# Kernel optimization log

Measured on AMD Instinct MI355X. Metric: run time of the kernel, lower is better.

## Reference

```python
import jax, jax.numpy as jnp
import numpy as np
import math

B, S, D, H = 2, 2048, 1024, 16
DPH = D // H  # 64

def setup_inputs() -> dict:
    key = jax.random.key(0)
    ks = jax.random.split(key, 13)
    scale = 1.0 / math.sqrt(D)
    inp = {
        'key': jax.random.normal(ks[0], (B, S, D), jnp.float32),
        'value': jax.random.normal(ks[1], (B, S, D), jnp.float32),
        'query': jax.random.normal(ks[2], (B, S, D), jnp.float32),
        # binary mask [B, q_len, k_len]; True = disallowed (masked_fill with -inf)
        'mask': jax.random.randint(ks[3], (B, S, S), 0, 2).astype(bool),
        'Wq': jax.random.normal(ks[4], (D, D), jnp.float32) * scale,
        'bq': jnp.zeros((D,), jnp.float32),
        'Wk': jax.random.normal(ks[5], (D, D), jnp.float32) * scale,
        'bk': jnp.zeros((D,), jnp.float32),
        'Wv': jax.random.normal(ks[6], (D, D), jnp.float32) * scale,
        'bv': jnp.zeros((D,), jnp.float32),
        'Wo': jax.random.normal(ks[7], (D, D), jnp.float32) * scale,
        'bo': jnp.zeros((D,), jnp.float32),
    }
    return inp

def _shape(x):
    # [B, S, D] -> [B, H, S, DPH]
    return x.reshape(B, -1, H, DPH).transpose(0, 2, 1, 3)

def reference(key, value, query, mask, Wq, bq, Wk, bk, Wv, bv, Wo, bo):
    k = _shape(key @ Wk + bk)      # [B,H,S,DPH]
    v = _shape(value @ Wv + bv)    # [B,H,S,DPH]
    q = _shape(query @ Wq + bq)    # [B,H,S,DPH]
    q = q / math.sqrt(DPH)
    scores = jnp.einsum('bhqd,bhkd->bhqk', q, k)   # [B,H,S,S]
    scores = jnp.where(mask[:, None, :, :], -jnp.inf, scores)
    attn = jax.nn.softmax(scores, axis=-1)
    # dropout is identity in eval / p=0
    ctx = jnp.einsum('bhqk,bhkd->bhqd', attn, v)   # [B,H,S,DPH]
    ctx = ctx.transpose(0, 2, 1, 3).reshape(B, -1, D)
    return ctx @ Wo + bo
```

## Files before the change

kernel.cpp:

```cpp
#include <hip/hip_runtime.h>
#include <hip/hip_bf16.h>
#include <cstdint>

#define B_   2
#define S_   2048
#define D_   1024
#define H_   16
#define DPH_ 64
#define NT_  (S_ / 64)

typedef float f32x4 __attribute__((ext_vector_type(4)));
typedef short bf16x8 __attribute__((ext_vector_type(8)));
typedef unsigned short u16;

static const size_t NE = (size_t)B_ * S_ * D_;
static const size_t DD = (size_t)D_ * D_;

__device__ __forceinline__ u16 f2bf(float f) {
  union { float f; unsigned u; } cv; cv.f = f;
  unsigned u = cv.u;
  return (u16)((u + 0x7fffu + ((u >> 16) & 1u)) >> 16);
}

__device__ __forceinline__ unsigned cvtpk(float a, float b) {
  unsigned r;
  asm("v_cvt_pk_bf16_f32 %0, %1, %2" : "=v"(r) : "v"(a), "v"(b));
  return r;
}

__device__ __forceinline__ void gld16(const void* g, void* l) {
  __builtin_amdgcn_global_load_lds((const __attribute__((address_space(1))) unsigned int*)g,
                                   (__attribute__((address_space(3))) unsigned int*)l, 16, 0, 0);
}

__global__ __launch_bounds__(256) void detect_mask_fmt(const uint4* __restrict__ m,
                                                       unsigned int* __restrict__ flags) {
  int i = blockIdx.x * 256 + threadIdx.x;
  uint4 v = m[i];
  int a = (v.x > 1u) | (v.y > 1u) | (v.z > 1u) | (v.w > 1u);
  int bb = ((v.x != 0u && v.x != 0x3f800000u) | (v.y != 0u && v.y != 0x3f800000u) |
            (v.z != 0u && v.z != 0x3f800000u) | (v.w != 0u && v.w != 0x3f800000u));
  int anyA = __any(a), anyB = __any(bb);
  if ((threadIdx.x & 63) == 0) {
    if (anyA) flags[0] = 1u;
    if (anyB) flags[1] = 1u;
  }
}

__device__ __forceinline__ unsigned nz4(unsigned w) {
  unsigned r = 0;
  if (w & 0x000000ffu) r |= 1u;
  if (w & 0x0000ff00u) r |= 2u;
  if (w & 0x00ff0000u) r |= 4u;
  if (w & 0xff000000u) r |= 8u;
  return r;
}

__global__ __launch_bounds__(256) void prep_bits(const void* __restrict__ src,
                                                 const unsigned int* __restrict__ flags,
                                                 unsigned long long* __restrict__ dst) {
  int i = blockIdx.x * 256 + threadIdx.x;
  unsigned long long w = 0;
  bool fourB = (flags[0] == 0u) || (flags[1] == 0u);
  if (fourB) {
    const uint4* p = (const uint4*)src + (size_t)i * 16;
#pragma unroll
    for (int j = 0; j < 16; ++j) {
      uint4 v = p[j];
      unsigned bits = (v.x ? 1u : 0u) | (v.y ? 2u : 0u) | (v.z ? 4u : 0u) | (v.w ? 8u : 0u);
      w |= (unsigned long long)bits << (j * 4);
    }
  } else {
    const uint4* p = (const uint4*)src + (size_t)i * 4;
#pragma unroll
    for (int j = 0; j < 4; ++j) {
      uint4 v = p[j];
      w |= (unsigned long long)nz4(v.x) << (j * 16 + 0);
      w |= (unsigned long long)nz4(v.y) << (j * 16 + 4);
      w |= (unsigned long long)nz4(v.z) << (j * 16 + 8);
      w |= (unsigned long long)nz4(v.w) << (j * 16 + 12);
    }
  }
  dst[i] = w;
}

__global__ __launch_bounds__(256) void cvt_w(const float* __restrict__ Wq, const float* __restrict__ Wk,
                                             const float* __restrict__ Wv, const float* __restrict__ Wo,
                                             u16* __restrict__ WT) {
  int idx2 = blockIdx.x;
  int mat = idx2 >> 9;
  const float* W = (mat == 0) ? Wq : (mat == 1) ? Wk : (mat == 2) ? Wv : Wo;
  u16* O = WT + (size_t)mat * DD;
  int t = (idx2 & 511) * 256 + threadIdx.x;
  int n = t & 1023, k8 = (t >> 10) << 3;
  bf16x8 o;
#pragma unroll
  for (int j = 0; j < 8; ++j) o[j] = (short)f2bf(W[(size_t)(k8 + j) * D_ + n]);
  *(bf16x8*)(O + (size_t)n * D_ + k8) = o;
}

struct GArgs {
  const void* A[3]; const u16* W[3]; const float* bias[3];
  void* C[3]; float scale[3]; int mode[3];
};

template <int AF32>
__global__ __launch_bounds__(256, 3) void gemm_bf16(GArgs ga) {
  __shared__ unsigned char smem[49152];
  constexpr int ABUF = AF32 ? 16384 : 8192;
  const int z = blockIdx.z;
  const u16* WT = ga.W[z]; const float* bias = ga.bias[z];
  void* Cout = ga.C[z]; const float scale = ga.scale[z]; const int mode = ga.mode[z];

  const int tid = threadIdx.x, wv = tid >> 6, lane = tid & 63;
  const int hi = lane >> 4, lo = lane & 15;
  const int wm = wv >> 1, wn = wv & 1;
  const int m0 = blockIdx.y * 128, n0 = blockIdx.x * 128;
  const char* ag = (const char*)ga.A[z] + (size_t)m0 * (AF32 ? 4096 : 2048);
  const char* bg = (const char*)WT + (size_t)n0 * 2048;
  unsigned char* sB0 = smem + 2 * ABUF;

  f32x4 acc[4][4];
#pragma unroll
  for (int i = 0; i < 4; ++i)
#pragma unroll
    for (int j = 0; j < 4; ++j) acc[i][j] = (f32x4){0.f, 0.f, 0.f, 0.f};

  auto stageA = [&](unsigned char* dst, int kt) {
    if constexpr (AF32) {
#pragma unroll
      for (int p = 0; p < 4; ++p) {
        int cid = p * 4 + wv;
        int slot = cid * 64 + lane;
        int r = slot >> 3, c = slot & 7;
        gld16(ag + (size_t)r * 4096 + kt * 128 + ((c ^ (r & 7)) * 16), dst + cid * 1024);
      }
    } else {
#pragma unroll
      for (int p = 0; p < 2; ++p) {
        int cid = p * 4 + wv;
        int slot = cid * 64 + lane;
        int r = slot >> 2, c = slot & 3;
        gld16(ag + (size_t)r * 2048 + kt * 64 + ((c ^ (r & 3)) * 16), dst + cid * 1024);
      }
    }
  };
  auto stageB = [&](unsigned char* dst, int kt) {
#pragma unroll
    for (int p = 0; p < 2; ++p) {
      int cid = p * 4 + wv;
      int slot = cid * 64 + lane;
      int r = slot >> 2, c = slot & 3;
      gld16(bg + (size_t)r * 2048 + kt * 64 + ((c ^ (r & 3)) * 16), dst + cid * 1024);
    }
  };

  stageA(smem, 0);
  stageB(sB0, 0);

  for (int kt = 0; kt < 32; ++kt) {
    int cur = kt & 1;
    unsigned char* sA = smem + cur * ABUF;
    unsigned char* sB = sB0 + cur * 8192;
    if (kt < 31) {
      stageA(smem + (cur ^ 1) * ABUF, kt + 1);
      stageB(sB0 + (cur ^ 1) * 8192, kt + 1);
      if constexpr (AF32) asm volatile("s_waitcnt vmcnt(6)" ::: "memory");
      else                asm volatile("s_waitcnt vmcnt(4)" ::: "memory");
    } else {
      asm volatile("s_waitcnt vmcnt(0)" ::: "memory");
    }
    __builtin_amdgcn_s_barrier();
    __builtin_amdgcn_sched_barrier(0);

    bf16x8 af[4], bf[4];
#pragma unroll
    for (int i = 0; i < 4; ++i) {
      int mr = 64 * wm + 16 * i + lo;
      if constexpr (AF32) {
        int s7 = mr & 7;
        f32x4 A0 = *(const f32x4*)(sA + mr * 128 + (((2 * hi) ^ s7) * 16));
        f32x4 A1 = *(const f32x4*)(sA + mr * 128 + (((2 * hi + 1) ^ s7) * 16));
        union { uint4 u; bf16x8 v; } cvu;
        cvu.u = make_uint4(cvtpk(A0[0], A0[1]), cvtpk(A0[2], A0[3]),
                           cvtpk(A1[0], A1[1]), cvtpk(A1[2], A1[3]));
        af[i] = cvu.v;
      } else {
        af[i] = *(const bf16x8*)(sA + mr * 64 + ((hi ^ (mr & 3)) * 16));
      }
      int nr = 64 * wn + 16 * i + lo;
      bf[i] = *(const bf16x8*)(sB + nr * 64 + ((hi ^ (nr & 3)) * 16));
    }
#pragma unroll
    for (int i = 0; i < 4; ++i)
#pragma unroll
      for (int j = 0; j < 4; ++j)
        acc[i][j] = __builtin_amdgcn_mfma_f32_16x16x32_bf16(af[i], bf[j], acc[i][j], 0, 0, 0);

    __builtin_amdgcn_sched_barrier(0);
    __builtin_amdgcn_s_barrier();
  }

  float bv[4];
#pragma unroll
  for (int j = 0; j < 4; ++j) bv[j] = bias[n0 + 64 * wn + 16 * j + lo];

  if (mode <= 1) {
#pragma unroll
    for (int i = 0; i < 4; ++i)
#pragma unroll
      for (int r = 0; r < 4; ++r) {
        int m = m0 + 64 * wm + 16 * i + 4 * hi + r;
#pragma unroll
        for (int j = 0; j < 4; ++j) {
          int n = n0 + 64 * wn + 16 * j + lo;
          float val = (acc[i][j][r] + bv[j]) * scale;
          if (mode == 0) ((u16*)Cout)[(size_t)m * D_ + n] = f2bf(val);
          else           ((float*)Cout)[(size_t)m * D_ + n] = val;
        }
      }
  } else {
    __syncthreads();
#pragma unroll
    for (int i = 0; i < 4; ++i) {
      int mb2 = 64 * wm + 16 * i + 4 * hi;
#pragma unroll
      for (int j = 0; j < 4; ++j) {
        int n = 64 * wn + 16 * j + lo;
        unsigned w0 = (unsigned)f2bf(acc[i][j][0] + bv[j]) | ((unsigned)f2bf(acc[i][j][1] + bv[j]) << 16);
        unsigned w1 = (unsigned)f2bf(acc[i][j][2] + bv[j]) | ((unsigned)f2bf(acc[i][j][3] + bv[j]) << 16);
        unsigned byteoff = n * 256 + ((2 * mb2) ^ ((n & 7) << 5));
        *(uint2*)(smem + byteoff) = make_uint2(w0, w1);
      }
    }
    __syncthreads();
    int nl = tid >> 1, half = tid & 1;
    unsigned ob[32];
#pragma unroll
    for (int s = 0; s < 16; ++s) {
      unsigned byteoff = nl * 256 + ((128 * half + 8 * s) ^ ((nl & 7) << 5));
      uint2 vv = *(const uint2*)(smem + byteoff);
      ob[2 * s] = vv.x; ob[2 * s + 1] = vv.y;
    }
    int bb = blockIdx.y >> 4;
    int habs = blockIdx.x * 2 + (nl >> 6);
    int dn = nl & 63;
    size_t sg = (size_t)(blockIdx.y & 15) * 128 + half * 64;
    u16* outp = (u16*)Cout + ((size_t)(bb * H_ + habs) * 64 + dn) * 2048 + sg;
#pragma unroll
    for (int c2 = 0; c2 < 8; ++c2)
      *(uint4*)(outp + c2 * 8) = *(uint4*)&ob[4 * c2];
  }
}

__global__ __launch_bounds__(256, 3) void attn_mfma3(const u16* __restrict__ Qb,
                                                     const u16* __restrict__ Kb,
                                                     const u16* __restrict__ VT,
                                                     const unsigned long long* __restrict__ M1,
                                                     u16* __restrict__ CTX) {
  __shared__ unsigned char sK[2][8192];
  __shared__ unsigned char sV[2][8192];
  __shared__ unsigned char sP[4][4096];
  const int tid = threadIdx.x, wv = tid >> 6, lane = tid & 63;
  const int hi = lane >> 4, lo = lane & 15;
  const int b = blockIdx.y >> 4, h = blockIdx.y & (H_ - 1);
  const int q0 = blockIdx.x * 128;
  const char* kg = (const char*)(Kb + (size_t)b * S_ * D_ + h * 64);
  const char* vg = (const char*)(VT + ((size_t)(b * H_ + h) * 64) * S_);
  unsigned* sPw = (unsigned*)sP[wv];

  const u16* qr0 = Qb + ((size_t)b * S_ + q0 + 32 * wv + lo) * D_ + h * 64;
  bf16x8 qa[2][2];
  qa[0][0] = *(const bf16x8*)(qr0 + 8 * hi);
  qa[0][1] = *(const bf16x8*)(qr0 + 32 + 8 * hi);
  qa[1][0] = *(const bf16x8*)(qr0 + (size_t)16 * D_ + 8 * hi);
  qa[1][1] = *(const bf16x8*)(qr0 + (size_t)16 * D_ + 32 + 8 * hi);

  auto stage8 = [&](unsigned char* dst, const char* srcbase, size_t rs) {
#pragma unroll
    for (int p = 0; p < 2; ++p) {
      int cid = p * 4 + wv;
      int slot = cid * 64 + lane;
      int r = slot >> 3, c = slot & 7;
      gld16(srcbase + (size_t)r * rs + ((c ^ (r & 7)) * 16), dst + cid * 1024);
    }
  };

  stage8(sK[0], kg, 2048);
  stage8(sV[0], vg, 4096);

  f32x4 acc[2][4];
#pragma unroll
  for (int hf = 0; hf < 2; ++hf)
#pragma unroll
    for (int i = 0; i < 4; ++i) acc[hf][i] = (f32x4){0.f, 0.f, 0.f, 0.f};
  float lrowp[2] = {0.f, 0.f};
  const unsigned long long* mrp = M1 + ((size_t)b * S_ + q0 + 32 * wv + lo) * NT_;

#define ATTN_STEP(CUR, KT)                                                             \
  {                                                                                    \
    if ((KT) < NT_ - 1) {                                                              \
      stage8(sK[(CUR) ^ 1], kg + (size_t)((KT) + 1) * 64 * 2048, 2048);                \
      stage8(sV[(CUR) ^ 1], vg + (size_t)((KT) + 1) * 128, 4096);                      \
      asm volatile("s_waitcnt vmcnt(4)" ::: "memory");                                 \
    } else {                                                                           \
      asm volatile("s_waitcnt vmcnt(0)" ::: "memory");                                 \
    }                                                                                  \
    __builtin_amdgcn_s_barrier();                                                      \
    __builtin_amdgcn_sched_barrier(0);                                                 \
    unsigned long long mwh0 = mrp[(KT)] >> (unsigned)(4 * hi);                         \
    unsigned long long mwh1 = mrp[(size_t)16 * NT_ + (KT)] >> (unsigned)(4 * hi);      \
    f32x4 sc[2][4];                                                                    \
    __builtin_amdgcn_s_setprio(1);                                                     \
    _Pragma("unroll")                                                                  \
    for (int nf = 0; nf < 4; ++nf) {                                                   \
      int key = 16 * nf + lo;                                                          \
      bf16x8 kb0 = *(const bf16x8*)(sK[(CUR)] + key * 128 + (((0 + hi) ^ (key & 7)) * 16)); \
      bf16x8 kb1 = *(const bf16x8*)(sK[(CUR)] + key * 128 + (((4 + hi) ^ (key & 7)) * 16)); \
      f32x4 z0 = (f32x4){0.f, 0.f, 0.f, 0.f};                                          \
      f32x4 z1 = (f32x4){0.f, 0.f, 0.f, 0.f};                                          \
      z0 = __builtin_amdgcn_mfma_f32_16x16x32_bf16(kb0, qa[0][0], z0, 0, 0, 0);        \
      z1 = __builtin_amdgcn_mfma_f32_16x16x32_bf16(kb0, qa[1][0], z1, 0, 0, 0);        \
      z0 = __builtin_amdgcn_mfma_f32_16x16x32_bf16(kb1, qa[0][1], z0, 0, 0, 0);        \
      z1 = __builtin_amdgcn_mfma_f32_16x16x32_bf16(kb1, qa[1][1], z1, 0, 0, 0);        \
      sc[0][nf] = z0; sc[1][nf] = z1;                                                  \
    }                                                                                  \
    __builtin_amdgcn_s_setprio(0);                                                     \
    _Pragma("unroll")                                                                  \
    for (int hf2 = 0; hf2 < 2; ++hf2) {                                                \
      unsigned long long mw = (hf2 == 0) ? mwh0 : mwh1;                                \
      unsigned nlo = ~(unsigned)mw;                                                    \
      unsigned nhi = ~(unsigned)(mw >> 32);                                            \
      float p[4][4];                                                                   \
      float rs = 0.f;                                                                  \
      _Pragma("unroll")                                                                \
      for (int nf = 0; nf < 4; ++nf) {                                                 \
        unsigned hfm = (nf < 2) ? nlo : nhi;                                           \
        _Pragma("unroll")                                                              \
        for (int r = 0; r < 4; ++r) {                                                  \
          float e = __builtin_amdgcn_exp2f(__builtin_fminf(sc[hf2][nf][r], 88.0f));    \
          int keep = ((int)(hfm << (31 - (16 * (nf & 1) + r)))) >> 31;                 \
          p[nf][r] = __uint_as_float(__float_as_uint(e) & (unsigned)keep);             \
        }                                                                              \
      }                                                                                \
      rs = ((p[0][0] + p[0][1]) + (p[0][2] + p[0][3])) +                               \
           ((p[1][0] + p[1][1]) + (p[1][2] + p[1][3])) +                               \
           ((p[2][0] + p[2][1]) + (p[2][2] + p[2][3])) +                               \
           ((p[3][0] + p[3][1]) + (p[3][2] + p[3][3]));                                \
      lrowp[hf2] += rs;                                                                \
      int rq = 16 * hf2 + lo;                                                          \
      _Pragma("unroll")                                                                \
      for (int nf = 0; nf < 4; ++nf) {                                                 \
        unsigned w0 = cvtpk(p[nf][0], p[nf][1]);                                       \
        unsigned w1 = cvtpk(p[nf][2], p[nf][3]);                                       \
        int dw = rq * 32 + ((8 * nf + 2 * hi) ^ ((lo & 7) << 2));                      \
        *(uint2*)(sPw + dw) = make_uint2(w0, w1);                                      \
      }                                                                                \
    }                                                                                  \
    __builtin_amdgcn_s_setprio(1);                                                     \
    _Pragma("unroll")                                                                  \
    for (int mh = 0; mh < 2; ++mh) {                                                   \
      bf16x8 pf0 = *(const bf16x8*)(sPw + (lo * 32 + ((16 * mh + 4 * hi) ^ ((lo & 7) << 2)))); \
      bf16x8 pf1 = *(const bf16x8*)(sPw + ((16 + lo) * 32 + ((16 * mh + 4 * hi) ^ ((lo & 7) << 2)))); \
      _Pragma("unroll")                                                                \
      for (int nd = 0; nd < 4; ++nd) {                                                 \
        int d = 16 * nd + lo;                                                          \
        bf16x8 vb = *(const bf16x8*)(sV[(CUR)] + d * 128 + (((4 * mh + hi) ^ (d & 7)) * 16)); \
        acc[0][nd] = __builtin_amdgcn_mfma_f32_16x16x32_bf16(vb, pf0, acc[0][nd], 0, 0, 0); \
        acc[1][nd] = __builtin_amdgcn_mfma_f32_16x16x32_bf16(vb, pf1, acc[1][nd], 0, 0, 0); \
      }                                                                                \
    }                                                                                  \
    __builtin_amdgcn_s_setprio(0);                                                     \
    __builtin_amdgcn_sched_barrier(0);                                                 \
    __builtin_amdgcn_s_barrier();                                                      \
  }

  for (int kt2 = 0; kt2 < NT_ / 2; ++kt2) {
    ATTN_STEP(0, 2 * kt2);
    ATTN_STEP(1, 2 * kt2 + 1);
  }
#undef ATTN_STEP

#pragma unroll
  for (int hf = 0; hf < 2; ++hf) {
    float lr = lrowp[hf];
    lr += __shfl_xor(lr, 16);
    lr += __shfl_xor(lr, 32);
    float inv = lr > 0.f ? 1.f / lr : 0.f;
    u16* crow = CTX + ((size_t)b * S_ + q0 + 32 * wv + 16 * hf + lo) * D_ + h * 64;
#pragma unroll
    for (int nd = 0; nd < 4; ++nd) {
      unsigned w0 = (unsigned)f2bf(acc[hf][nd][0] * inv) | ((unsigned)f2bf(acc[hf][nd][1] * inv) << 16);
      unsigned w1 = (unsigned)f2bf(acc[hf][nd][2] * inv) | ((unsigned)f2bf(acc[hf][nd][3] * inv) << 16);
      *(uint2*)(crow + 16 * nd + 4 * hi) = make_uint2(w0, w1);
    }
  }
}

extern "C" void kernel_launch(void* const* d_in, const int* in_sizes, int n_in,
                              void* d_out, int out_size, void* d_ws, size_t ws_size,
                              hipStream_t stream) {
  const float* key   = (const float*)d_in[0];
  const float* value = (const float*)d_in[1];
  const float* query = (const float*)d_in[2];
  const void*  mask  = d_in[3];
  const float* Wq = (const float*)d_in[4];
  const float* bq = (const float*)d_in[5];
  const float* Wk = (const float*)d_in[6];
  const float* bk = (const float*)d_in[7];
  const float* Wv = (const float*)d_in[8];
  const float* bv = (const float*)d_in[9];
  const float* Wo = (const float*)d_in[10];
  const float* bo = (const float*)d_in[11];

  u16* Qb  = (u16*)d_ws;
  u16* Kb  = Qb + NE;
  u16* VTb = Kb + NE;
  u16* WT  = VTb + NE;
  unsigned long long* M1 = (unsigned long long*)(WT + 4 * DD);
  unsigned int* flags = (unsigned int*)(M1 + (size_t)B_ * S_ * NT_);

  hipMemsetAsync(flags, 0, 8, stream);
  detect_mask_fmt<<<128, 256, 0, stream>>>((const uint4*)mask, flags);
  prep_bits<<<512, 256, 0, stream>>>(mask, flags, M1);
  cvt_w<<<2048, 256, 0, stream>>>(Wq, Wk, Wv, Wo, WT);

  const float QSCALE = 0.125f * 1.4426950408889634f;
  GArgs g3;
  g3.A[0] = query; g3.W[0] = WT + 0 * DD; g3.bias[0] = bq; g3.C[0] = Qb;  g3.scale[0] = QSCALE; g3.mode[0] = 0;
  g3.A[1] = key;   g3.W[1] = WT + 1 * DD; g3.bias[1] = bk; g3.C[1] = Kb;  g3.scale[1] = 1.f;    g3.mode[1] = 0;
  g3.A[2] = value; g3.W[2] = WT + 2 * DD; g3.bias[2] = bv; g3.C[2] = VTb; g3.scale[2] = 1.f;    g3.mode[2] = 2;
  gemm_bf16<1><<<dim3(D_ / 128, (B_ * S_) / 128, 3), 256, 0, stream>>>(g3);

  attn_mfma3<<<dim3(S_ / 128, B_ * H_), 256, 0, stream>>>(Qb, Kb, VTb, M1, Qb);

  GArgs go;
  go.A[0] = Qb; go.W[0] = WT + 3 * DD; go.bias[0] = bo; go.C[0] = d_out; go.scale[0] = 1.f; go.mode[0] = 1;
  go.A[1] = Qb; go.W[1] = WT + 3 * DD; go.bias[1] = bo; go.C[1] = d_out; go.scale[1] = 1.f; go.mode[1] = 1;
  go.A[2] = Qb; go.W[2] = WT + 3 * DD; go.bias[2] = bo; go.C[2] = d_out; go.scale[2] = 1.f; go.mode[2] = 1;
  gemm_bf16<0><<<dim3(D_ / 128, (B_ * S_) / 128, 1), 256, 0, stream>>>(go);
}
```

Baseline: 301.5 us.

## Halve attention query tile to 64 rows and swap GEMM grid rasterization

The attention kernel now processes 64 queries per block (16 per wave) instead of 128, shrinking registers and the P shared buffer so launch bounds can target 4 blocks per CU, and doubling the grid size. This aims to improve occupancy and load balance across CUs at the cost of staging each K/V tile twice as often per query. The projection GEMMs swap grid x/y so consecutive blocks iterate over M rows rather than N columns, changing L2 reuse of weights versus activations.

```diff
diff --git a/kernel.cpp b/kernel.cpp
--- a/kernel.cpp
+++ b/kernel.cpp
@@ -115,7 +115,7 @@
   const int tid = threadIdx.x, wv = tid >> 6, lane = tid & 63;
   const int hi = lane >> 4, lo = lane & 15;
   const int wm = wv >> 1, wn = wv & 1;
-  const int m0 = blockIdx.y * 128, n0 = blockIdx.x * 128;
+  const int m0 = blockIdx.x * 128, n0 = blockIdx.y * 128;
   const char* ag = (const char*)ga.A[z] + (size_t)m0 * (AF32 ? 4096 : 2048);
   const char* bg = (const char*)WT + (size_t)n0 * 2048;
   unsigned char* sB0 = smem + 2 * ABUF;
@@ -242,10 +242,10 @@
       uint2 vv = *(const uint2*)(smem + byteoff);
       ob[2 * s] = vv.x; ob[2 * s + 1] = vv.y;
     }
-    int bb = blockIdx.y >> 4;
-    int habs = blockIdx.x * 2 + (nl >> 6);
+    int bb = blockIdx.x >> 4;
+    int habs = blockIdx.y * 2 + (nl >> 6);
     int dn = nl & 63;
-    size_t sg = (size_t)(blockIdx.y & 15) * 128 + half * 64;
+    size_t sg = (size_t)(blockIdx.x & 15) * 128 + half * 64;
     u16* outp = (u16*)Cout + ((size_t)(bb * H_ + habs) * 64 + dn) * 2048 + sg;
 #pragma unroll
     for (int c2 = 0; c2 < 8; ++c2)
@@ -253,28 +253,25 @@
   }
 }
 
-__global__ __launch_bounds__(256, 3) void attn_mfma3(const u16* __restrict__ Qb,
+__global__ __launch_bounds__(256, 4) void attn_mfma4(const u16* __restrict__ Qb,
                                                      const u16* __restrict__ Kb,
                                                      const u16* __restrict__ VT,
                                                      const unsigned long long* __restrict__ M1,
                                                      u16* __restrict__ CTX) {
   __shared__ unsigned char sK[2][8192];
   __shared__ unsigned char sV[2][8192];
-  __shared__ unsigned char sP[4][4096];
+  __shared__ unsigned char sP[4][2048];
   const int tid = threadIdx.x, wv = tid >> 6, lane = tid & 63;
   const int hi = lane >> 4, lo = lane & 15;
   const int b = blockIdx.y >> 4, h = blockIdx.y & (H_ - 1);
-  const int q0 = blockIdx.x * 128;
+  const int q0 = blockIdx.x * 64;
   const char* kg = (const char*)(Kb + (size_t)b * S_ * D_ + h * 64);
   const char* vg = (const char*)(VT + ((size_t)(b * H_ + h) * 64) * S_);
   unsigned* sPw = (unsigned*)sP[wv];
 
-  const u16* qr0 = Qb + ((size_t)b * S_ + q0 + 32 * wv + lo) * D_ + h * 64;
-  bf16x8 qa[2][2];
-  qa[0][0] = *(const bf16x8*)(qr0 + 8 * hi);
-  qa[0][1] = *(const bf16x8*)(qr0 + 32 + 8 * hi);
-  qa[1][0] = *(const bf16x8*)(qr0 + (size_t)16 * D_ + 8 * hi);
-  qa[1][1] = *(const bf16x8*)(qr0 + (size_t)16 * D_ + 32 + 8 * hi);
+  const u16* qr0 = Qb + ((size_t)b * S_ + q0 + 16 * wv + lo) * D_ + h * 64;
+  bf16x8 qa0 = *(const bf16x8*)(qr0 + 8 * hi);
+  bf16x8 qa1 = *(const bf16x8*)(qr0 + 32 + 8 * hi);
 
   auto stage8 = [&](unsigned char* dst, const char* srcbase, size_t rs) {
 #pragma unroll
@@ -289,13 +286,11 @@
   stage8(sK[0], kg, 2048);
   stage8(sV[0], vg, 4096);
 
-  f32x4 acc[2][4];
-#pragma unroll
-  for (int hf = 0; hf < 2; ++hf)
-#pragma unroll
-    for (int i = 0; i < 4; ++i) acc[hf][i] = (f32x4){0.f, 0.f, 0.f, 0.f};
-  float lrowp[2] = {0.f, 0.f};
-  const unsigned long long* mrp = M1 + ((size_t)b * S_ + q0 + 32 * wv + lo) * NT_;
+  f32x4 acc[4];
+#pragma unroll
+  for (int i = 0; i < 4; ++i) acc[i] = (f32x4){0.f, 0.f, 0.f, 0.f};
+  float lrowp = 0.f;
+  const unsigned long long* mrp = M1 + ((size_t)b * S_ + q0 + 16 * wv + lo) * NT_;
 
 #define ATTN_STEP(CUR, KT)                                                             \
   {                                                                                    \
@@ -308,66 +303,53 @@
     }                                                                                  \
     __builtin_amdgcn_s_barrier();                                                      \
     __builtin_amdgcn_sched_barrier(0);                                                 \
-    unsigned long long mwh0 = mrp[(KT)] >> (unsigned)(4 * hi);                         \
-    unsigned long long mwh1 = mrp[(size_t)16 * NT_ + (KT)] >> (unsigned)(4 * hi);      \
-    f32x4 sc[2][4];                                                                    \
+    unsigned long long mw = mrp[(KT)] >> (unsigned)(4 * hi);                           \
+    f32x4 sc[4];                                                                       \
     __builtin_amdgcn_s_setprio(1);                                                     \
     _Pragma("unroll")                                                                  \
     for (int nf = 0; nf < 4; ++nf) {                                                   \
       int key = 16 * nf + lo;                                                          \
       bf16x8 kb0 = *(const bf16x8*)(sK[(CUR)] + key * 128 + (((0 + hi) ^ (key & 7)) * 16)); \
       bf16x8 kb1 = *(const bf16x8*)(sK[(CUR)] + key * 128 + (((4 + hi) ^ (key & 7)) * 16)); \
-      f32x4 z0 = (f32x4){0.f, 0.f, 0.f, 0.f};                                          \
-      f32x4 z1 = (f32x4){0.f, 0.f, 0.f, 0.f};                                          \
-      z0 = __builtin_amdgcn_mfma_f32_16x16x32_bf16(kb0, qa[0][0], z0, 0, 0, 0);        \
-      z1 = __builtin_amdgcn_mfma_f32_16x16x32_bf16(kb0, qa[1][0], z1, 0, 0, 0);        \
-      z0 = __builtin_amdgcn_mfma_f32_16x16x32_bf16(kb1, qa[0][1], z0, 0, 0, 0);        \
-      z1 = __builtin_amdgcn_mfma_f32_16x16x32_bf16(kb1, qa[1][1], z1, 0, 0, 0);        \
-      sc[0][nf] = z0; sc[1][nf] = z1;                                                  \
+      f32x4 z = (f32x4){0.f, 0.f, 0.f, 0.f};                                           \
+      z = __builtin_amdgcn_mfma_f32_16x16x32_bf16(kb0, qa0, z, 0, 0, 0);               \
+      z = __builtin_amdgcn_mfma_f32_16x16x32_bf16(kb1, qa1, z, 0, 0, 0);               \
+      sc[nf] = z;                                                                      \
     }                                                                                  \
     __builtin_amdgcn_s_setprio(0);                                                     \
+    unsigned nlo = ~(unsigned)mw;                                                      \
+    unsigned nhi = ~(unsigned)(mw >> 32);                                              \
+    float p[4][4];                                                                     \
     _Pragma("unroll")                                                                  \
-    for (int hf2 = 0; hf2 < 2; ++hf2) {                                                \
-      unsigned long long mw = (hf2 == 0) ? mwh0 : mwh1;                                \
-      unsigned nlo = ~(unsigned)mw;                                                    \
-      unsigned nhi = ~(unsigned)(mw >> 32);                                            \
-      float p[4][4];                                                                   \
-      float rs = 0.f;                                                                  \
+    for (int nf = 0; nf < 4; ++nf) {                                                   \
+      unsigned hfm = (nf < 2) ? nlo : nhi;                                             \
       _Pragma("unroll")                                                                \
-      for (int nf = 0; nf < 4; ++nf) {                                                 \
-        unsigned hfm = (nf < 2) ? nlo : nhi;                                           \
-        _Pragma("unroll")                                                              \
-        for (int r = 0; r < 4; ++r) {                                                  \
-          float e = __builtin_amdgcn_exp2f(__builtin_fminf(sc[hf2][nf][r], 88.0f));    \
-          int keep = ((int)(hfm << (31 - (16 * (nf & 1) + r)))) >> 31;                 \
-          p[nf][r] = __uint_as_float(__float_as_uint(e) & (unsigned)keep);             \
-        }                                                                              \
+      for (int r = 0; r < 4; ++r) {                                                    \
+        float e = __builtin_amdgcn_exp2f(__builtin_fminf(sc[nf][r], 88.0f));           \
+        int keep = ((int)(hfm << (31 - (16 * (nf & 1) + r)))) >> 31;                   \
+        p[nf][r] = __uint_as_float(__float_as_uint(e) & (unsigned)keep);               \
       }                                                                                \
-      rs = ((p[0][0] + p[0][1]) + (p[0][2] + p[0][3])) +                               \
-           ((p[1][0] + p[1][1]) + (p[1][2] + p[1][3])) +                               \
-           ((p[2][0] + p[2][1]) + (p[2][2] + p[2][3])) +                               \
-           ((p[3][0] + p[3][1]) + (p[3][2] + p[3][3]));                                \
-      lrowp[hf2] += rs;                                                                \
-      int rq = 16 * hf2 + lo;                                                          \
-      _Pragma("unroll")                                                                \
-      for (int nf = 0; nf < 4; ++nf) {                                                 \
-        unsigned w0 = cvtpk(p[nf][0], p[nf][1]);                                       \
-        unsigned w1 = cvtpk(p[nf][2], p[nf][3]);                                       \
-        int dw = rq * 32 + ((8 * nf + 2 * hi) ^ ((lo & 7) << 2));                      \
-        *(uint2*)(sPw + dw) = make_uint2(w0, w1);                                      \
-      }                                                                                \
+    }                                                                                  \
+    lrowp += ((p[0][0] + p[0][1]) + (p[0][2] + p[0][3])) +                             \
+             ((p[1][0] + p[1][1]) + (p[1][2] + p[1][3])) +                             \
+             ((p[2][0] + p[2][1]) + (p[2][2] + p[2][3])) +                             \
+             ((p[3][0] + p[3][1]) + (p[3][2] + p[3][3]));                              \
+    _Pragma("unroll")                                                                  \
+    for (int nf = 0; nf < 4; ++nf) {                                                   \
+      unsigned w0 = cvtpk(p[nf][0], p[nf][1]);                                         \
+      unsigned w1 = cvtpk(p[nf][2], p[nf][3]);                                         \
+      int dw = lo * 32 + ((8 * nf + 2 * hi) ^ ((lo & 7) << 2));                        \
+      *(uint2*)(sPw + dw) = make_uint2(w0, w1);                                        \
     }                                                                                  \
     __builtin_amdgcn_s_setprio(1);                                                     \
     _Pragma("unroll")                                                                  \
     for (int mh = 0; mh < 2; ++mh) {                                                   \
-      bf16x8 pf0 = *(const bf16x8*)(sPw + (lo * 32 + ((16 * mh + 4 * hi) ^ ((lo & 7) << 2)))); \
-      bf16x8 pf1 = *(const bf16x8*)(sPw + ((16 + lo) * 32 + ((16 * mh + 4 * hi) ^ ((lo & 7) << 2)))); \
+      bf16x8 pf = *(const bf16x8*)(sPw + (lo * 32 + ((16 * mh + 4 * hi) ^ ((lo & 7) << 2)))); \
       _Pragma("unroll")                                                                \
       for (int nd = 0; nd < 4; ++nd) {                                                 \
         int d = 16 * nd + lo;                                                          \
         bf16x8 vb = *(const bf16x8*)(sV[(CUR)] + d * 128 + (((4 * mh + hi) ^ (d & 7)) * 16)); \
-        acc[0][nd] = __builtin_amdgcn_mfma_f32_16x16x32_bf16(vb, pf0, acc[0][nd], 0, 0, 0); \
-        acc[1][nd] = __builtin_amdgcn_mfma_f32_16x16x32_bf16(vb, pf1, acc[1][nd], 0, 0, 0); \
+        acc[nd] = __builtin_amdgcn_mfma_f32_16x16x32_bf16(vb, pf, acc[nd], 0, 0, 0);   \
       }                                                                                \
     }                                                                                  \
     __builtin_amdgcn_s_setprio(0);                                                     \
@@ -381,19 +363,16 @@
   }
 #undef ATTN_STEP
 
-#pragma unroll
-  for (int hf = 0; hf < 2; ++hf) {
-    float lr = lrowp[hf];
-    lr += __shfl_xor(lr, 16);
-    lr += __shfl_xor(lr, 32);
-    float inv = lr > 0.f ? 1.f / lr : 0.f;
-    u16* crow = CTX + ((size_t)b * S_ + q0 + 32 * wv + 16 * hf + lo) * D_ + h * 64;
-#pragma unroll
-    for (int nd = 0; nd < 4; ++nd) {
-      unsigned w0 = (unsigned)f2bf(acc[hf][nd][0] * inv) | ((unsigned)f2bf(acc[hf][nd][1] * inv) << 16);
-      unsigned w1 = (unsigned)f2bf(acc[hf][nd][2] * inv) | ((unsigned)f2bf(acc[hf][nd][3] * inv) << 16);
-      *(uint2*)(crow + 16 * nd + 4 * hi) = make_uint2(w0, w1);
-    }
+  float lr = lrowp;
+  lr += __shfl_xor(lr, 16);
+  lr += __shfl_xor(lr, 32);
+  float inv = lr > 0.f ? 1.f / lr : 0.f;
+  u16* crow = CTX + ((size_t)b * S_ + q0 + 16 * wv + lo) * D_ + h * 64;
+#pragma unroll
+  for (int nd = 0; nd < 4; ++nd) {
+    unsigned w0 = (unsigned)f2bf(acc[nd][0] * inv) | ((unsigned)f2bf(acc[nd][1] * inv) << 16);
+    unsigned w1 = (unsigned)f2bf(acc[nd][2] * inv) | ((unsigned)f2bf(acc[nd][3] * inv) << 16);
+    *(uint2*)(crow + 16 * nd + 4 * hi) = make_uint2(w0, w1);
   }
 }
 
@@ -430,13 +409,13 @@
   g3.A[0] = query; g3.W[0] = WT + 0 * DD; g3.bias[0] = bq; g3.C[0] = Qb;  g3.scale[0] = QSCALE; g3.mode[0] = 0;
   g3.A[1] = key;   g3.W[1] = WT + 1 * DD; g3.bias[1] = bk; g3.C[1] = Kb;  g3.scale[1] = 1.f;    g3.mode[1] = 0;
   g3.A[2] = value; g3.W[2] = WT + 2 * DD; g3.bias[2] = bv; g3.C[2] = VTb; g3.scale[2] = 1.f;    g3.mode[2] = 2;
-  gemm_bf16<1><<<dim3(D_ / 128, (B_ * S_) / 128, 3), 256, 0, stream>>>(g3);
-
-  attn_mfma3<<<dim3(S_ / 128, B_ * H_), 256, 0, stream>>>(Qb, Kb, VTb, M1, Qb);
+  gemm_bf16<1><<<dim3((B_ * S_) / 128, D_ / 128, 3), 256, 0, stream>>>(g3);
+
+  attn_mfma4<<<dim3(S_ / 64, B_ * H_), 256, 0, stream>>>(Qb, Kb, VTb, M1, Qb);
 
   GArgs go;
   go.A[0] = Qb; go.W[0] = WT + 3 * DD; go.bias[0] = bo; go.C[0] = d_out; go.scale[0] = 1.f; go.mode[0] = 1;
   go.A[1] = Qb; go.W[1] = WT + 3 * DD; go.bias[1] = bo; go.C[1] = d_out; go.scale[1] = 1.f; go.mode[1] = 1;
   go.A[2] = Qb; go.W[2] = WT + 3 * DD; go.bias[2] = bo; go.C[2] = d_out; go.scale[2] = 1.f; go.mode[2] = 1;
-  gemm_bf16<0><<<dim3(D_ / 128, (B_ * S_) / 128, 1), 256, 0, stream>>>(go);
-}
+  gemm_bf16<0><<<dim3((B_ * S_) / 128, D_ / 128, 1), 256, 0, stream>>>(go);
+}
```

New measurement: 282.6 us. 6.3% less time.
